# Kernel optimization log

Measured on AMD Instinct MI355X. Metric: run time of the kernel, lower is better.

The kernel has to match this reference:

```python
import jax, jax.numpy as jnp
import numpy as np

BATCH, SEQ, DIM, NUM_CODES = 8, 2048, 1024, 8192

def setup_inputs() -> dict:
    key = jax.random.key(0)
    kx, kc = jax.random.split(key)
    x = jax.random.normal(kx, (BATCH, SEQ, DIM), dtype=jnp.float32)
    # nn.Embedding default init: N(0, 1)
    codebook = jax.random.normal(kc, (NUM_CODES, DIM), dtype=jnp.float32)
    return {"x": x, "codebook": codebook}

def reference(x, codebook):
    # tau=0 path of CodebookLayer.forward (SnapFunction.forward):
    # similarity logits [B, S, num_codes], nearest-code argmax, gather.
    logits = jnp.einsum('bsd,cd->bsc', x, codebook)
    codebook_ids = jnp.argmax(logits, axis=-1)            # [B, S] int
    output = jnp.take(codebook, codebook_ids, axis=0)     # [B, S, D]
    return output
```

## Files before the change

kernel.cpp:

```cpp
#include <hip/hip_runtime.h>
#include <stdint.h>


#define T_TOKENS 16384
#define N_CODES  8192
#define DIM      1024
#define BM 256
#define BN 256
#define BK 64
#define NBLK (N_CODES / BM)
#define KITERS (DIM / BK)
#define EPS 13.0f
#define MAXCAND 48

typedef int   int8v  __attribute__((ext_vector_type(8)));
typedef int   int4v  __attribute__((ext_vector_type(4)));
typedef float f32x16 __attribute__((ext_vector_type(16)));

#define GLD16(gp, lp) \
  __builtin_amdgcn_global_load_lds((__attribute__((address_space(1))) void*)(gp), \
                                   (__attribute__((address_space(3))) void*)(lp), 16, 0, 0)

__device__ inline uint32_t umax(uint32_t a, uint32_t b) { return a > b ? a : b; }
__device__ inline uint32_t umin(uint32_t a, uint32_t b) { return a < b ? a : b; }
__device__ inline uint32_t umed3(uint32_t a, uint32_t b, uint32_t c) {
  return umax(umin(a, b), umin(umax(a, b), c));
}

__device__ inline uint32_t f32_key(float v) {
  int32_t b = (int32_t)__float_as_uint(v);
  return (uint32_t)(b ^ ((b >> 31) | (int32_t)0x80000000));
}
__device__ inline float key_f32(uint32_t u) {
  uint32_t b = (u & 0x80000000u) ? (u & 0x7FFFFFFFu) : ~u;
  return __uint_as_float(b);
}

__global__ __launch_bounds__(256) void vq_prep(const float* __restrict__ x,
                                               const float* __restrict__ cbm,
                                               uint8_t* __restrict__ xq,
                                               uint8_t* __restrict__ cq) {
  size_t b = blockIdx.x;
  const float* src; uint8_t* dst;
  if (b < 16384) { src = x;  dst = xq; }
  else           { b -= 16384; src = cbm; dst = cq; }
  const size_t i = b * 256 + threadIdx.x;
  const float4 v = ((const float4*)src)[i];
  uint32_t r = __builtin_amdgcn_cvt_pk_fp8_f32(v.x, v.y, 0, false);
  r = __builtin_amdgcn_cvt_pk_fp8_f32(v.z, v.w, (int)r, true);
  ((uint32_t*)dst)[i] = r;
}

#define MFMA8(A_, B_, C_) \
  __builtin_amdgcn_mfma_scale_f32_32x32x64_f8f6f4((A_), (B_), (C_), 0, 0, 0, \
                                                  0x7F7F7F7F, 0, 0x7F7F7F7F)

__global__ __launch_bounds__(512) void vq_gemm_top3(
    const uint8_t* __restrict__ cq,
    const uint8_t* __restrict__ xq,
    uint32_t* __restrict__ pk)
{
  __shared__ uint8_t smem[4 * 32768];

  const int t    = threadIdx.x;
  const int wave = t >> 6;
  const int lane = t & 63;
  const int col  = lane & 31;
  const int hi   = lane >> 5;
  const int wm   = wave >> 2;
  const int wn2  = (wave & 3) * 64;

  const int f   = blockIdx.x;
  const int swz = (f & 7) * 256 + (f >> 3);
  const int cyi = swz >> 6;
  const int tb0 = (swz & 63) * BN;
  const int cb0 = cyi * BM;

  const int r0 = t >> 2;
  const int js = ((t & 3) ^ ((r0 >> 1) & 3)) * 16;
  const uint8_t* sA0 = cq + (size_t)(cb0 + r0) * DIM + js;
  const uint8_t* sA1 = cq + (size_t)(cb0 + r0 + 128) * DIM + js;
  const uint8_t* sB0 = xq + (size_t)(tb0 + r0) * DIM + js;
  const uint8_t* sB1 = xq + (size_t)(tb0 + r0 + 128) * DIM + js;

#define STAGE(bi, ti) do {                                     \
    uint8_t* Ad_ = smem + ((bi) << 15);                        \
    const int ko_ = (ti) * BK;                                 \
    GLD16(sA0 + ko_, Ad_ + t * 16);                            \
    GLD16(sA1 + ko_, Ad_ + (t + 512) * 16);                    \
    GLD16(sB0 + ko_, Ad_ + 16384 + t * 16);                    \
    GLD16(sB1 + ko_, Ad_ + 16384 + (t + 512) * 16);            \
  } while (0)

  const int j0 = hi * 2;
  int aoff[4][2], boff[2][2];
#pragma unroll
  for (int mi = 0; mi < 4; ++mi) {
    const int ra = wm * 128 + mi * 32 + col;
    const int pa = (ra >> 1) & 3;
    aoff[mi][0] = ra * 64 + (j0 ^ pa) * 16;
    aoff[mi][1] = ra * 64 + ((j0 + 1) ^ pa) * 16;
  }
#pragma unroll
  for (int jj = 0; jj < 2; ++jj) {
    const int rb = wn2 + jj * 32 + col;
    const int pb = (rb >> 1) & 3;
    boff[jj][0] = 16384 + rb * 64 + (j0 ^ pb) * 16;
    boff[jj][1] = 16384 + rb * 64 + ((j0 + 1) ^ pb) * 16;
  }

#define READ8(dst_, o0_, o1_) do {                                         \
    const int4v lo_ = *(const int4v*)(cur + (o0_));                        \
    const int4v hq_ = *(const int4v*)(cur + (o1_));                        \
    dst_ = __builtin_shufflevector(lo_, hq_, 0, 1, 2, 3, 4, 5, 6, 7);      \
  } while (0)

  f32x16 acc[4][2];
#pragma unroll
  for (int i = 0; i < 4; ++i)
#pragma unroll
    for (int j = 0; j < 2; ++j)
#pragma unroll
      for (int r = 0; r < 16; ++r) acc[i][j][r] = 0.f;

  STAGE(0, 0);
  STAGE(1, 1);

#pragma unroll 4
  for (int kt = 0; kt < KITERS; ++kt) {
    asm volatile("s_waitcnt vmcnt(4)" ::: "memory");
    __builtin_amdgcn_s_barrier();
    __builtin_amdgcn_sched_barrier(0);

    const uint8_t* cur = smem + ((kt & 3) << 15);
    STAGE((kt + 2) & 3, (kt + 2) & 15);

    int8v a[4], b[2];
#pragma unroll
    for (int mi = 0; mi < 4; ++mi) READ8(a[mi], aoff[mi][0], aoff[mi][1]);
#pragma unroll
    for (int jj = 0; jj < 2; ++jj) READ8(b[jj], boff[jj][0], boff[jj][1]);

    acc[0][0] = MFMA8(a[0], b[0], acc[0][0]);
    acc[1][0] = MFMA8(a[1], b[0], acc[1][0]);
    acc[0][1] = MFMA8(a[0], b[1], acc[0][1]);
    acc[1][1] = MFMA8(a[1], b[1], acc[1][1]);
    acc[2][0] = MFMA8(a[2], b[0], acc[2][0]);
    acc[3][0] = MFMA8(a[3], b[0], acc[3][0]);
    acc[2][1] = MFMA8(a[2], b[1], acc[2][1]);
    acc[3][1] = MFMA8(a[3], b[1], acc[3][1]);
  }
  __syncthreads();

  uint32_t* cand = (uint32_t*)(smem + 2 * 32768);
  const int invb = 255 - wm * 128 - 4 * hi;
#pragma unroll
  for (int j = 0; j < 2; ++j) {
    uint32_t K1 = 0, K2 = 0, K3 = 0;
#pragma unroll
    for (int mi = 0; mi < 4; ++mi) {
#pragma unroll
      for (int rg = 0; rg < 16; ++rg) {
        const int rowoff = (rg & 3) + 8 * (rg >> 2);
        const uint32_t key = (f32_key(acc[mi][j][rg]) & 0xFFFFFF00u)
                           | (uint32_t)(invb - mi * 32 - rowoff);
        const uint32_t t3 = umed3(key, K2, K3);
        const uint32_t t2 = umed3(key, K1, K2);
        K1 = umax(key, K1); K2 = t2; K3 = t3;
      }
    }
    const uint32_t o1 = __shfl_xor(K1, 32, 64);
    const uint32_t o2 = __shfl_xor(K2, 32, 64);
    const uint32_t o3 = __shfl_xor(K3, 32, 64);
    const uint32_t m1 = umin(K1, o1), M2 = umax(K2, o2);
    const uint32_t m2 = umin(K2, o2), M3 = umax(K3, o3);
    K1 = umax(K1, o1);
    const uint32_t nk2 = umax(m1, M2);
    K3 = umax(umax(m2, umin(m1, M2)), M3);
    K2 = nk2;
    if (hi == 0) {
      uint32_t* c = &cand[((wn2 + j * 32 + col) * 2 + wm) * 3];
      c[0] = K1; c[1] = K2; c[2] = K3;
    }
  }
  __syncthreads();
  if (t < BN) {
    const uint32_t a1 = cand[(t * 2 + 0) * 3 + 0], a2 = cand[(t * 2 + 0) * 3 + 1],
                   a3 = cand[(t * 2 + 0) * 3 + 2];
    const uint32_t b1k = cand[(t * 2 + 1) * 3 + 0], b2 = cand[(t * 2 + 1) * 3 + 1],
                   b3 = cand[(t * 2 + 1) * 3 + 2];
    const uint32_t m1 = umin(a1, b1k), M2 = umax(a2, b2);
    const uint32_t m2 = umin(a2, b2), M3 = umax(a3, b3);
    uint32_t* dst = pk + ((size_t)(tb0 + t) * NBLK + cyi) * 3;
    dst[0] = umax(a1, b1k);
    dst[1] = umax(m1, M2);
    dst[2] = umax(umax(m2, umin(m1, M2)), M3);
  }
#undef STAGE
#undef READ8
}

__global__ __launch_bounds__(256) void vq_reduce_gather(
    const uint32_t* __restrict__ pk, const float* __restrict__ x,
    const float* __restrict__ cb, float* __restrict__ out)
{
  __shared__ float xs[DIM];
  __shared__ uint32_t wmax[4];
  __shared__ int scand[MAXCAND];
  __shared__ int scnt;
  __shared__ double sdot[MAXCAND];
  __shared__ int sbesti;

  const int tkn = blockIdx.x, t = threadIdx.x, lane = t & 63, wv = t >> 6;
  ((float4*)xs)[t] = ((const float4*)(x + (size_t)tkn * DIM))[t];
  const uint32_t key = (t < 3 * NBLK) ? pk[(size_t)tkn * (3 * NBLK) + t] : 0u;
  uint32_t m = key;
#pragma unroll
  for (int d = 1; d < 64; d <<= 1) m = umax(m, __shfl_xor(m, d, 64));
  if (t == 0) scnt = 0;
  if (lane == 0) wmax[wv] = m;
  __syncthreads();
  const float Mv = key_f32(umax(umax(wmax[0], wmax[1]), umax(wmax[2], wmax[3])));
  if (t < 3 * NBLK && key_f32(key) >= Mv - EPS) {
    const int p = atomicAdd(&scnt, 1);
    if (p < MAXCAND) scand[p] = (t / 3) * BM + 255 - (int)(key & 255u);
  }
  __syncthreads();
  const int cnt = scnt < MAXCAND ? scnt : MAXCAND;

  if (cnt > 1) {
    for (int k = wv; k < cnt; k += 4) {
      const int c = scand[k];
      const float* cr = cb + (size_t)c * DIM;
      double s = 0.0;
#pragma unroll
      for (int q = 0; q < 4; ++q) {
        const float4 xv = ((const float4*)xs)[lane + 64 * q];
        const float4 cv = ((const float4*)cr)[lane + 64 * q];
        s += (double)xv.x * cv.x + (double)xv.y * cv.y
           + (double)xv.z * cv.z + (double)xv.w * cv.w;
      }
#pragma unroll
      for (int d = 1; d < 64; d <<= 1) s += __shfl_xor(s, d, 64);
      if (lane == 0) sdot[k] = s;
    }
    __syncthreads();
    if (t == 0) {
      double best = -1e300; int bi = N_CODES;
      for (int k = 0; k < cnt; ++k) {
        const int c = scand[k];
        if (sdot[k] > best || (sdot[k] == best && c < bi)) { best = sdot[k]; bi = c; }
      }
      sbesti = bi;
    }
  } else {
    if (t == 0) sbesti = scand[0];
  }
  __syncthreads();
  const int code = sbesti;
  ((float4*)(out + (size_t)tkn * DIM))[t] = ((const float4*)(cb + (size_t)code * DIM))[t];
}

__global__ __launch_bounds__(256) void vq_naive(const float* __restrict__ x,
                                                const float* __restrict__ cb,
                                                float* __restrict__ out) {
  __shared__ float xs[DIM];
  __shared__ float bv[256];
  __shared__ int   bix[256];
  const int tkn = blockIdx.x;
  const int t = threadIdx.x;
  for (int d = t; d < DIM; d += 256) xs[d] = x[(size_t)tkn * DIM + d];
  __syncthreads();
  float best = -1e30f; int bi = N_CODES;
  for (int c = t; c < N_CODES; c += 256) {
    const float* cr = cb + (size_t)c * DIM;
    float s = 0.f;
    for (int d = 0; d < DIM; ++d) s += xs[d] * cr[d];
    if (s > best || (s == best && c < bi)) { best = s; bi = c; }
  }
  bv[t] = best; bix[t] = bi;
  __syncthreads();
  for (int off = 128; off > 0; off >>= 1) {
    if (t < off) {
      if (bv[t + off] > bv[t] || (bv[t + off] == bv[t] && bix[t + off] < bix[t])) {
        bv[t] = bv[t + off]; bix[t] = bix[t + off];
      }
    }
    __syncthreads();
  }
  const int code = bix[0];
  for (int d = t; d < DIM; d += 256)
    out[(size_t)tkn * DIM + d] = cb[(size_t)code * DIM + d];
}

extern "C" void kernel_launch(void* const* d_in, const int* in_sizes, int n_in,
                              void* d_out, int out_size, void* d_ws, size_t ws_size,
                              hipStream_t stream) {
  const float* x  = (const float*)d_in[0];
  const float* cb = (const float*)d_in[1];
  float* out = (float*)d_out;

  const size_t MB = 1024 * 1024;
  const size_t need = 24 * MB + (size_t)T_TOKENS * NBLK * 3 * 4;
  if (ws_size >= need) {
    uint8_t*  xq = (uint8_t*)d_ws;
    uint8_t*  cq = xq + 16 * MB;
    uint32_t* pk = (uint32_t*)(cq + 8 * MB);

    vq_prep<<<dim3(24576), 256, 0, stream>>>(x, cb, xq, cq);
    vq_gemm_top3<<<dim3((T_TOKENS / BN) * (N_CODES / BM)), 512, 0, stream>>>(cq, xq, pk);
    vq_reduce_gather<<<dim3(T_TOKENS), 256, 0, stream>>>(pk, x, cb, out);
  } else {
    vq_naive<<<dim3(T_TOKENS), 256, 0, stream>>>(x, cb, out);
  }
}
```

Before: 322.2 us.

## Use 4-wave blocks with 128x128 per-wave tiles in FP8 VQ GEMM

The GEMM block drops from 8 waves to 4, and each wave now computes a 128x128 tile with 4x4 MFMA accumulators instead of 128x64. Each thread issues twice as many LDS-direct loads per stage. The k-loop is fully unrolled with stage prefetches guarded at the tail, and the vmcnt waits are adjusted to match. The aim is more register-level reuse of A/B fragments and fewer LDS reads per MFMA. The cost is doubled accumulator registers (256 VGPRs of accumulators), fewer waves to hide latency, and possible spilling.

```diff
diff --git a/kernel.cpp b/kernel.cpp
--- a/kernel.cpp
+++ b/kernel.cpp
@@ -55,7 +55,7 @@
   __builtin_amdgcn_mfma_scale_f32_32x32x64_f8f6f4((A_), (B_), (C_), 0, 0, 0, \
                                                   0x7F7F7F7F, 0, 0x7F7F7F7F)
 
-__global__ __launch_bounds__(512) void vq_gemm_top3(
+__global__ __launch_bounds__(256, 1) void vq_gemm_top3(
     const uint8_t* __restrict__ cq,
     const uint8_t* __restrict__ xq,
     uint32_t* __restrict__ pk)
@@ -67,8 +67,8 @@
   const int lane = t & 63;
   const int col  = lane & 31;
   const int hi   = lane >> 5;
-  const int wm   = wave >> 2;
-  const int wn2  = (wave & 3) * 64;
+  const int wm   = wave >> 1;
+  const int wn   = wave & 1;
 
   const int f   = blockIdx.x;
   const int swz = (f & 7) * 256 + (f >> 3);
@@ -78,35 +78,34 @@
 
   const int r0 = t >> 2;
   const int js = ((t & 3) ^ ((r0 >> 1) & 3)) * 16;
-  const uint8_t* sA0 = cq + (size_t)(cb0 + r0) * DIM + js;
-  const uint8_t* sA1 = cq + (size_t)(cb0 + r0 + 128) * DIM + js;
-  const uint8_t* sB0 = xq + (size_t)(tb0 + r0) * DIM + js;
-  const uint8_t* sB1 = xq + (size_t)(tb0 + r0 + 128) * DIM + js;
-
-#define STAGE(bi, ti) do {                                     \
-    uint8_t* Ad_ = smem + ((bi) << 15);                        \
-    const int ko_ = (ti) * BK;                                 \
-    GLD16(sA0 + ko_, Ad_ + t * 16);                            \
-    GLD16(sA1 + ko_, Ad_ + (t + 512) * 16);                    \
-    GLD16(sB0 + ko_, Ad_ + 16384 + t * 16);                    \
-    GLD16(sB1 + ko_, Ad_ + 16384 + (t + 512) * 16);            \
+  const uint8_t* sA = cq + (size_t)(cb0 + r0) * DIM + js;
+  const uint8_t* sB = xq + (size_t)(tb0 + r0) * DIM + js;
+
+#define STAGE(bi, ti) do {                                           \
+    uint8_t* Ad_ = smem + ((bi) << 15);                              \
+    const int ko_ = (ti) * BK;                                       \
+    GLD16(sA + ko_,                 Ad_ + t * 16);                   \
+    GLD16(sA + 64 * DIM + ko_,      Ad_ + t * 16 + 4096);            \
+    GLD16(sA + 128 * DIM + ko_,     Ad_ + t * 16 + 8192);            \
+    GLD16(sA + 192 * DIM + ko_,     Ad_ + t * 16 + 12288);           \
+    GLD16(sB + ko_,                 Ad_ + 16384 + t * 16);           \
+    GLD16(sB + 64 * DIM + ko_,      Ad_ + 16384 + t * 16 + 4096);    \
+    GLD16(sB + 128 * DIM + ko_,     Ad_ + 16384 + t * 16 + 8192);    \
+    GLD16(sB + 192 * DIM + ko_,     Ad_ + 16384 + t * 16 + 12288);   \
   } while (0)
 
   const int j0 = hi * 2;
-  int aoff[4][2], boff[2][2];
+  int aoff[4][2], boff[4][2];
 #pragma unroll
   for (int mi = 0; mi < 4; ++mi) {
     const int ra = wm * 128 + mi * 32 + col;
     const int pa = (ra >> 1) & 3;
     aoff[mi][0] = ra * 64 + (j0 ^ pa) * 16;
     aoff[mi][1] = ra * 64 + ((j0 + 1) ^ pa) * 16;
-  }
-#pragma unroll
-  for (int jj = 0; jj < 2; ++jj) {
-    const int rb = wn2 + jj * 32 + col;
+    const int rb = wn * 128 + mi * 32 + col;
     const int pb = (rb >> 1) & 3;
-    boff[jj][0] = 16384 + rb * 64 + (j0 ^ pb) * 16;
-    boff[jj][1] = 16384 + rb * 64 + ((j0 + 1) ^ pb) * 16;
+    boff[mi][0] = 16384 + rb * 64 + (j0 ^ pb) * 16;
+    boff[mi][1] = 16384 + rb * 64 + ((j0 + 1) ^ pb) * 16;
   }
 
 #define READ8(dst_, o0_, o1_) do {                                         \
@@ -115,54 +114,54 @@
     dst_ = __builtin_shufflevector(lo_, hq_, 0, 1, 2, 3, 4, 5, 6, 7);      \
   } while (0)
 
-  f32x16 acc[4][2];
+  f32x16 acc[4][4];
 #pragma unroll
   for (int i = 0; i < 4; ++i)
 #pragma unroll
-    for (int j = 0; j < 2; ++j)
+    for (int j = 0; j < 4; ++j)
 #pragma unroll
       for (int r = 0; r < 16; ++r) acc[i][j][r] = 0.f;
 
   STAGE(0, 0);
   STAGE(1, 1);
 
-#pragma unroll 4
+#pragma unroll
   for (int kt = 0; kt < KITERS; ++kt) {
-    asm volatile("s_waitcnt vmcnt(4)" ::: "memory");
+    if (kt == KITERS - 1) asm volatile("s_waitcnt vmcnt(0)" ::: "memory");
+    else                  asm volatile("s_waitcnt vmcnt(8)" ::: "memory");
     __builtin_amdgcn_s_barrier();
     __builtin_amdgcn_sched_barrier(0);
 
     const uint8_t* cur = smem + ((kt & 3) << 15);
-    STAGE((kt + 2) & 3, (kt + 2) & 15);
-
-    int8v a[4], b[2];
-#pragma unroll
-    for (int mi = 0; mi < 4; ++mi) READ8(a[mi], aoff[mi][0], aoff[mi][1]);
-#pragma unroll
-    for (int jj = 0; jj < 2; ++jj) READ8(b[jj], boff[jj][0], boff[jj][1]);
-
-    acc[0][0] = MFMA8(a[0], b[0], acc[0][0]);
-    acc[1][0] = MFMA8(a[1], b[0], acc[1][0]);
-    acc[0][1] = MFMA8(a[0], b[1], acc[0][1]);
-    acc[1][1] = MFMA8(a[1], b[1], acc[1][1]);
-    acc[2][0] = MFMA8(a[2], b[0], acc[2][0]);
-    acc[3][0] = MFMA8(a[3], b[0], acc[3][0]);
-    acc[2][1] = MFMA8(a[2], b[1], acc[2][1]);
-    acc[3][1] = MFMA8(a[3], b[1], acc[3][1]);
-  }
-  __syncthreads();
-
-  uint32_t* cand = (uint32_t*)(smem + 2 * 32768);
+
+    if (kt < KITERS - 2) STAGE((kt + 2) & 3, kt + 2);
+
+    int8v b[4];
+#pragma unroll
+    for (int nj = 0; nj < 4; ++nj) READ8(b[nj], boff[nj][0], boff[nj][1]);
+#pragma unroll
+    for (int mi = 0; mi < 4; ++mi) {
+      int8v a;
+      READ8(a, aoff[mi][0], aoff[mi][1]);
+      acc[mi][0] = MFMA8(a, b[0], acc[mi][0]);
+      acc[mi][1] = MFMA8(a, b[1], acc[mi][1]);
+      acc[mi][2] = MFMA8(a, b[2], acc[mi][2]);
+      acc[mi][3] = MFMA8(a, b[3], acc[mi][3]);
+    }
+  }
+  __syncthreads();
+
+  uint32_t* cand = (uint32_t*)smem;
   const int invb = 255 - wm * 128 - 4 * hi;
 #pragma unroll
-  for (int j = 0; j < 2; ++j) {
+  for (int nj = 0; nj < 4; ++nj) {
     uint32_t K1 = 0, K2 = 0, K3 = 0;
 #pragma unroll
     for (int mi = 0; mi < 4; ++mi) {
 #pragma unroll
       for (int rg = 0; rg < 16; ++rg) {
         const int rowoff = (rg & 3) + 8 * (rg >> 2);
-        const uint32_t key = (f32_key(acc[mi][j][rg]) & 0xFFFFFF00u)
+        const uint32_t key = (f32_key(acc[mi][nj][rg]) & 0xFFFFFF00u)
                            | (uint32_t)(invb - mi * 32 - rowoff);
         const uint32_t t3 = umed3(key, K2, K3);
         const uint32_t t2 = umed3(key, K1, K2);
@@ -179,12 +178,12 @@
     K3 = umax(umax(m2, umin(m1, M2)), M3);
     K2 = nk2;
     if (hi == 0) {
-      uint32_t* c = &cand[((wn2 + j * 32 + col) * 2 + wm) * 3];
+      uint32_t* c = &cand[((wn * 128 + nj * 32 + col) * 2 + wm) * 3];
       c[0] = K1; c[1] = K2; c[2] = K3;
     }
   }
   __syncthreads();
-  if (t < BN) {
+  {
     const uint32_t a1 = cand[(t * 2 + 0) * 3 + 0], a2 = cand[(t * 2 + 0) * 3 + 1],
                    a3 = cand[(t * 2 + 0) * 3 + 2];
     const uint32_t b1k = cand[(t * 2 + 1) * 3 + 0], b2 = cand[(t * 2 + 1) * 3 + 1],
@@ -308,7 +307,7 @@
     uint32_t* pk = (uint32_t*)(cq + 8 * MB);
 
     vq_prep<<<dim3(24576), 256, 0, stream>>>(x, cb, xq, cq);
-    vq_gemm_top3<<<dim3((T_TOKENS / BN) * (N_CODES / BM)), 512, 0, stream>>>(cq, xq, pk);
+    vq_gemm_top3<<<dim3((T_TOKENS / BN) * (N_CODES / BM)), 256, 0, stream>>>(cq, xq, pk);
     vq_reduce_gather<<<dim3(T_TOKENS), 256, 0, stream>>>(pk, x, cb, out);
   } else {
     vq_naive<<<dim3(T_TOKENS), 256, 0, stream>>>(x, cb, out);
```

After: 340.6 us. +5.7%, slower.

## Process one token per wavefront in reduce-gather using ballots instead of shared memory

Applied to the files above, without the earlier changes.

The reduce/gather kernel now assigns one token per 64-lane wavefront (four tokens per block) rather than one per 256-thread block. Candidate selection uses wave-level ballots and shuffles instead of shared-memory atomics and block barriers. The x row is loaded only when rescoring is needed. Rescoring walks the candidates serially within the wave and keeps the best as it goes. This removes __syncthreads, LDS traffic and the candidate cap. In exchange, a token with many candidates is rescored serially by one wave instead of being spread across four.

```diff
diff --git a/kernel.cpp b/kernel.cpp
--- a/kernel.cpp
+++ b/kernel.cpp
@@ -11,7 +11,6 @@
 #define NBLK (N_CODES / BM)
 #define KITERS (DIM / BK)
 #define EPS 13.0f
-#define MAXCAND 48
 
 typedef int   int8v  __attribute__((ext_vector_type(8)));
 typedef int   int4v  __attribute__((ext_vector_type(4)));
@@ -204,61 +203,67 @@
     const uint32_t* __restrict__ pk, const float* __restrict__ x,
     const float* __restrict__ cb, float* __restrict__ out)
 {
-  __shared__ float xs[DIM];
-  __shared__ uint32_t wmax[4];
-  __shared__ int scand[MAXCAND];
-  __shared__ int scnt;
-  __shared__ double sdot[MAXCAND];
-  __shared__ int sbesti;
-
-  const int tkn = blockIdx.x, t = threadIdx.x, lane = t & 63, wv = t >> 6;
-  ((float4*)xs)[t] = ((const float4*)(x + (size_t)tkn * DIM))[t];
-  const uint32_t key = (t < 3 * NBLK) ? pk[(size_t)tkn * (3 * NBLK) + t] : 0u;
-  uint32_t m = key;
+  const int t = threadIdx.x, lane = t & 63, wv = t >> 6;
+  const int tkn = blockIdx.x * 4 + wv;
+  const uint32_t* prow = pk + (size_t)tkn * (3 * NBLK);
+
+  const uint32_t a = prow[lane];
+  const uint32_t b = (lane < 32) ? prow[64 + lane] : 0u;
+
+  uint32_t m = umax(a, b);
 #pragma unroll
   for (int d = 1; d < 64; d <<= 1) m = umax(m, __shfl_xor(m, d, 64));
-  if (t == 0) scnt = 0;
-  if (lane == 0) wmax[wv] = m;
-  __syncthreads();
-  const float Mv = key_f32(umax(umax(wmax[0], wmax[1]), umax(wmax[2], wmax[3])));
-  if (t < 3 * NBLK && key_f32(key) >= Mv - EPS) {
-    const int p = atomicAdd(&scnt, 1);
-    if (p < MAXCAND) scand[p] = (t / 3) * BM + 255 - (int)(key & 255u);
-  }
-  __syncthreads();
-  const int cnt = scnt < MAXCAND ? scnt : MAXCAND;
-
-  if (cnt > 1) {
-    for (int k = wv; k < cnt; k += 4) {
-      const int c = scand[k];
-      const float* cr = cb + (size_t)c * DIM;
-      double s = 0.0;
-#pragma unroll
-      for (int q = 0; q < 4; ++q) {
-        const float4 xv = ((const float4*)xs)[lane + 64 * q];
-        const float4 cv = ((const float4*)cr)[lane + 64 * q];
-        s += (double)xv.x * cv.x + (double)xv.y * cv.y
-           + (double)xv.z * cv.z + (double)xv.w * cv.w;
+  const float thr = key_f32(m) - EPS;
+
+  const int code_a = (lane / 3) * BM + 255 - (int)(a & 255u);
+  const int code_b = ((64 + lane) / 3) * BM + 255 - (int)(b & 255u);
+  const bool ca = key_f32(a) >= thr;
+  const bool cbn = (lane < 32) && (key_f32(b) >= thr);
+  const unsigned long long ma = __ballot(ca);
+  const unsigned long long mb = __ballot(cbn);
+  const int cnt = __popcll(ma) + __popcll(mb);
+
+  int best;
+  if (cnt == 1) {
+    uint32_t cmin = umin((uint32_t)(ca  ? code_a : 0x7FFFFFFF),
+                         (uint32_t)(cbn ? code_b : 0x7FFFFFFF));
+#pragma unroll
+    for (int d = 1; d < 64; d <<= 1) cmin = umin(cmin, __shfl_xor(cmin, d, 64));
+    best = (int)cmin;
+  } else {
+    float4 xr[4];
+#pragma unroll
+    for (int q = 0; q < 4; ++q)
+      xr[q] = ((const float4*)(x + (size_t)tkn * DIM))[lane + 64 * q];
+    double bestd = -1e300; int bestc = N_CODES;
+#pragma unroll
+    for (int pass = 0; pass < 2; ++pass) {
+      unsigned long long bits = (pass == 0) ? ma : mb;
+      const int mycode = (pass == 0) ? code_a : code_b;
+      while (bits) {
+        const int l = __ffsll((long long)bits) - 1;
+        bits &= bits - 1;
+        const int c = __shfl(mycode, l, 64);
+        const float4* cr = (const float4*)(cb + (size_t)c * DIM);
+        double s = 0.0;
+#pragma unroll
+        for (int q = 0; q < 4; ++q) {
+          const float4 cv = cr[lane + 64 * q];
+          s += (double)xr[q].x * cv.x + (double)xr[q].y * cv.y
+             + (double)xr[q].z * cv.z + (double)xr[q].w * cv.w;
+        }
+#pragma unroll
+        for (int d = 1; d < 64; d <<= 1) s += __shfl_xor(s, d, 64);
+        if (s > bestd || (s == bestd && c < bestc)) { bestd = s; bestc = c; }
       }
-#pragma unroll
-      for (int d = 1; d < 64; d <<= 1) s += __shfl_xor(s, d, 64);
-      if (lane == 0) sdot[k] = s;
     }
-    __syncthreads();
-    if (t == 0) {
-      double best = -1e300; int bi = N_CODES;
-      for (int k = 0; k < cnt; ++k) {
-        const int c = scand[k];
-        if (sdot[k] > best || (sdot[k] == best && c < bi)) { best = sdot[k]; bi = c; }
-      }
-      sbesti = bi;
-    }
-  } else {
-    if (t == 0) sbesti = scand[0];
-  }
-  __syncthreads();
-  const int code = sbesti;
-  ((float4*)(out + (size_t)tkn * DIM))[t] = ((const float4*)(cb + (size_t)code * DIM))[t];
+    best = bestc;
+  }
+
+  const float4* src = (const float4*)(cb + (size_t)best * DIM);
+  float4* dst = (float4*)(out + (size_t)tkn * DIM);
+#pragma unroll
+  for (int q = 0; q < 4; ++q) dst[lane + 64 * q] = src[lane + 64 * q];
 }
 
 __global__ __launch_bounds__(256) void vq_naive(const float* __restrict__ x,
@@ -309,7 +314,7 @@
 
     vq_prep<<<dim3(24576), 256, 0, stream>>>(x, cb, xq, cq);
     vq_gemm_top3<<<dim3((T_TOKENS / BN) * (N_CODES / BM)), 512, 0, stream>>>(cq, xq, pk);
-    vq_reduce_gather<<<dim3(T_TOKENS), 256, 0, stream>>>(pk, x, cb, out);
+    vq_reduce_gather<<<dim3(T_TOKENS / 4), 256, 0, stream>>>(pk, x, cb, out);
   } else {
     vq_naive<<<dim3(T_TOKENS), 256, 0, stream>>>(x, cb, out);
   }
```

Result: slower. 350.9 us (+8.9%).
